# Kernel optimization log

Measured on AMD Instinct MI355X. Metric: run time of the kernel, lower is better.

## Reference

```python
import jax, jax.numpy as jnp
import numpy as np
import math

HEAD = 4
D_MODEL = 128
N_NODES = 2048
SEQ_LEN = 1
D_K = D_MODEL // HEAD
BATCH = 64


def conv1x1_relu(x, w, b):
    # x: [B, C, N, L], w: [O, C], b: [O]  (1x1 Conv2d + ReLU; dropout is identity in eval)
    return jax.nn.relu(jnp.einsum('oc,bcnl->bonl', w, x) + b[None, :, None, None])


def setup_inputs() -> dict:
    key = jax.random.key(0)
    ks = jax.random.split(key, 12)
    s = 0.05
    return {
        'x': jax.random.normal(ks[0], (BATCH, D_MODEL, N_NODES, SEQ_LEN), jnp.float32),
        'q_w': jax.random.normal(ks[1], (D_MODEL, D_MODEL), jnp.float32) * s,
        'q_b': jnp.zeros((D_MODEL,), jnp.float32),
        'v_w': jax.random.normal(ks[2], (D_MODEL, D_MODEL), jnp.float32) * s,
        'v_b': jnp.zeros((D_MODEL,), jnp.float32),
        'c_w': jax.random.normal(ks[3], (D_MODEL, D_MODEL), jnp.float32) * s,
        'c_b': jnp.zeros((D_MODEL,), jnp.float32),
        'memory': jax.random.normal(ks[4], (HEAD, SEQ_LEN, N_NODES, D_K), jnp.float32) * s,
        'nodevec1': jax.random.normal(ks[5], (N_NODES, 10), jnp.float32),
        'nodevec2': jax.random.normal(ks[6], (10, N_NODES), jnp.float32),
        'weights_pool': jax.random.normal(ks[7], (SEQ_LEN, 3, 3), jnp.float32) * s,
        'bias_pool': jax.random.normal(ks[8], (N_NODES, D_K), jnp.float32) * s,
        'aff_w': jnp.ones((D_MODEL, N_NODES, SEQ_LEN), jnp.float32),
        'aff_b': jnp.zeros((D_MODEL, N_NODES, SEQ_LEN), jnp.float32),
    }


def reference(x, q_w, q_b, v_w, v_b, c_w, c_b, memory, nodevec1, nodevec2,
              weights_pool, bias_pool, aff_w, aff_b):
    B = x.shape[0]
    scale = math.sqrt(D_K)

    query = conv1x1_relu(x, q_w, q_b)
    value = conv1x1_relu(x, v_w, v_b)

    # [B, d_model, N, L] -> [B, h, d_k, N, L] -> [B, h, L, N, d_k]
    def split_heads(t):
        return t.reshape(B, HEAD, D_K, N_NODES, SEQ_LEN).transpose(0, 1, 4, 3, 2)

    query = split_heads(query)
    value = split_heads(value)

    key_ = jax.nn.softmax(memory / scale, axis=-1)      # [h, L, N, d_k]
    query = jax.nn.softmax(query / scale, axis=-1)      # [B, h, L, N, d_k]

    Aapt = jax.nn.softmax(jax.nn.relu(nodevec1 @ nodevec2), axis=-1)  # [N, N]

    kv = jnp.einsum('hlnx,bhlny->bhlxy', key_, value)          # [B,h,L,d_k,d_k]
    attn_qkv = jnp.einsum('bhlnx,bhlxy->bhlny', query, kv)     # [B,h,L,N,d_k]

    weights = jnp.einsum('nm,dio->nio', Aapt, weights_pool)    # [N,3,3]
    bias_dyn = Aapt @ bias_pool                                # [N,d_k]
    attn_dyn = jnp.einsum('bhlnc,nio->bhlnc', value, weights) + bias_dyn[None, None, None, :, :]

    out = attn_qkv + attn_dyn                                  # [B,h,L,N,d_k]
    out = out.transpose(0, 1, 4, 3, 2).reshape(B, D_MODEL, N_NODES, SEQ_LEN)
    out = conv1x1_relu(out, c_w, c_b)

    # num_nodes (2048) not in [170, 358, 5] -> affine-residual branch runs
    out = out * aff_w[None] + aff_b[None] + out
    return out
```

## Files before the change

kernel.cpp:

```cpp
#include <hip/hip_runtime.h>

#define NB 64
#define CH 128
#define NNODE 2048
#define NH 4
#define DKK 32
#define INVS 0.17677669529663687f

typedef __bf16 bf16x8 __attribute__((ext_vector_type(8)));
typedef float f32x4 __attribute__((ext_vector_type(4)));
typedef unsigned short ushort_t;

union U16x8 { uint4 u; bf16x8 b; unsigned short s[8]; };
union U16x4 { uint2 u; unsigned short s[4]; };

__device__ inline bf16x8 as_bf16x8(uint4 u){ U16x8 x; x.u = u; return x.b; }
__device__ inline unsigned short f2b(float f){ __bf16 h = (__bf16)f; return __builtin_bit_cast(unsigned short, h); }
__device__ inline float b2f(unsigned short u){ __bf16 h = __builtin_bit_cast(__bf16, u); return (float)h; }

#define SWZ_IDX(n, c) ((n) * 128 + ((c) ^ ((((n) >> 2) & 7) << 3)))

__global__ __launch_bounds__(256) void kA(const float* __restrict__ qw,
    const float* __restrict__ vw, const float* __restrict__ cw,
    const float* __restrict__ memory, const float* __restrict__ bias_pool,
    ushort_t* __restrict__ wqb, ushort_t* __restrict__ wvb, ushort_t* __restrict__ wcb,
    ushort_t* __restrict__ keysT, float* __restrict__ bias_dyn,
    ushort_t* __restrict__ bpT,
    const float* __restrict__ nv1, const float* __restrict__ nv2,
    ushort_t* __restrict__ Ebuf)
{
  __shared__ float red[4];
  int tid = threadIdx.x;
  if (blockIdx.x < 256) {
    int gid = blockIdx.x * 256 + tid;
    if (gid < 16384) { wqb[gid] = f2b(qw[gid]); wvb[gid] = f2b(vw[gid]); wcb[gid] = f2b(cw[gid]); }
    bias_dyn[gid] = 0.f;
    { int k = gid >> 11, m = gid & 2047;
      bpT[gid] = f2b(bias_pool[m * 32 + k]); }
    if (gid < 8192) {
      int h = gid >> 11, n = gid & 2047;
      const float* src = memory + (size_t)gid * 32;
      float v[32]; float m = -1e30f;
      #pragma unroll
      for (int i = 0; i < 32; ++i) { v[i] = src[i] * INVS; m = fmaxf(m, v[i]); }
      float s = 0.f;
      #pragma unroll
      for (int i = 0; i < 32; ++i) { v[i] = __expf(v[i] - m); s += v[i]; }
      float inv = 1.f / s;
      #pragma unroll
      for (int i = 0; i < 32; ++i)
        keysT[(size_t)(h * 32 + i) * 2048 + n] = f2b(v[i] * inv);
    }
  } else {
    int n = blockIdx.x - 256;
    float a1[10];
    #pragma unroll
    for (int d = 0; d < 10; ++d) a1[d] = nv1[n * 10 + d];
    int m0 = tid * 8;
    float s[8];
    #pragma unroll
    for (int j = 0; j < 8; ++j) s[j] = 0.f;
    #pragma unroll
    for (int d = 0; d < 10; ++d) {
      const float* p = nv2 + d * 2048 + m0;
      float4 u = *(const float4*)p; float4 v = *(const float4*)(p + 4);
      s[0] += a1[d] * u.x; s[1] += a1[d] * u.y; s[2] += a1[d] * u.z; s[3] += a1[d] * u.w;
      s[4] += a1[d] * v.x; s[5] += a1[d] * v.y; s[6] += a1[d] * v.z; s[7] += a1[d] * v.w;
    }
    float e[8]; float sum = 0.f;
    #pragma unroll
    for (int j = 0; j < 8; ++j) { e[j] = __expf(fmaxf(s[j], 0.f)); sum += e[j]; }
    #pragma unroll
    for (int d = 1; d < 64; d <<= 1) sum += __shfl_xor(sum, d);
    if ((tid & 63) == 0) red[tid >> 6] = sum;
    __syncthreads();
    float inv = 1.f / (red[0] + red[1] + red[2] + red[3]);
    U16x8 o;
    #pragma unroll
    for (int j = 0; j < 8; ++j) o.s[j] = f2b(e[j] * inv);
    *(uint4*)(Ebuf + (size_t)n * 2048 + m0) = o.u;
  }
}

__global__ __launch_bounds__(256, 5) void kB(
    const ushort_t* __restrict__ Ebuf, const ushort_t* __restrict__ bpT,
    float* __restrict__ bias_dyn,
    const float* __restrict__ x,
    const ushort_t* __restrict__ wqb, const ushort_t* __restrict__ wvb,
    const float* __restrict__ qbias, const float* __restrict__ vbias,
    const ushort_t* __restrict__ keysT,
    ushort_t* __restrict__ QsT, ushort_t* __restrict__ VT,
    float* __restrict__ kvp)
{
  __shared__ __align__(16) ushort_t XT[64 * 128];
  __shared__ __align__(16) ushort_t QO[64 * 128];
  int tid = threadIdx.x; int wv = tid >> 6; int lane = tid & 63;
  int quad = lane >> 4; int l16 = lane & 15;
  f32x4 zero4 = {0.f,0.f,0.f,0.f};

  if (blockIdx.x < 128) {
    int bid = blockIdx.x;
    int n0 = (bid >> 3) * 128;
    int m0 = (bid & 7) * 256;
    int r0 = n0 + 32 * wv;
    f32x4 acc[2][2];
    acc[0][0] = zero4; acc[0][1] = zero4; acc[1][0] = zero4; acc[1][1] = zero4;
    for (int ks = 0; ks < 256; ks += 32) {
      int mb = m0 + ks + 8 * quad;
      bf16x8 a0 = *(const bf16x8*)(Ebuf + (size_t)(r0 + l16) * 2048 + mb);
      bf16x8 a1 = *(const bf16x8*)(Ebuf + (size_t)(r0 + 16 + l16) * 2048 + mb);
      bf16x8 b0 = *(const bf16x8*)(bpT + (size_t)l16 * 2048 + mb);
      bf16x8 b1 = *(const bf16x8*)(bpT + (size_t)(16 + l16) * 2048 + mb);
      acc[0][0] = __builtin_amdgcn_mfma_f32_16x16x32_bf16(a0, b0, acc[0][0], 0, 0, 0);
      acc[0][1] = __builtin_amdgcn_mfma_f32_16x16x32_bf16(a0, b1, acc[0][1], 0, 0, 0);
      acc[1][0] = __builtin_amdgcn_mfma_f32_16x16x32_bf16(a1, b0, acc[1][0], 0, 0, 0);
      acc[1][1] = __builtin_amdgcn_mfma_f32_16x16x32_bf16(a1, b1, acc[1][1], 0, 0, 0);
    }
    #pragma unroll
    for (int rt = 0; rt < 2; ++rt)
      #pragma unroll
      for (int ct = 0; ct < 2; ++ct)
        #pragma unroll
        for (int r = 0; r < 4; ++r)
          atomicAdd(bias_dyn + (size_t)(r0 + 16*rt + 4*quad + r) * 32 + 16*ct + l16,
                    acc[rt][ct][r]);
    return;
  }

  int bid = blockIdx.x - 128; int b = bid >> 5; int n0 = (bid & 31) * 64;

  uint4 wq[2][4];
  #pragma unroll
  for (int ct = 0; ct < 2; ++ct)
    #pragma unroll
    for (int k0 = 0; k0 < 4; ++k0)
      wq[ct][k0] = *(const uint4*)(wqb + (32 * wv + 16 * ct + l16) * 128 + 32 * k0 + 8 * quad);

  {
    float4 r[8];
    int n4 = 4 * (tid & 15);
    #pragma unroll
    for (int p = 0; p < 2; ++p) {
      int c4 = 4 * ((tid >> 4) + 16 * p);
      #pragma unroll
      for (int j = 0; j < 4; ++j)
        r[4 * p + j] = *(const float4*)(x + (size_t)(b * 128 + c4 + j) * 2048 + n0 + n4);
    }
    #pragma unroll
    for (int p = 0; p < 2; ++p) {
      int c4 = 4 * ((tid >> 4) + 16 * p);
      #pragma unroll
      for (int i = 0; i < 4; ++i) {
        U16x4 w;
        w.s[0] = f2b(((const float*)&r[4 * p + 0])[i]);
        w.s[1] = f2b(((const float*)&r[4 * p + 1])[i]);
        w.s[2] = f2b(((const float*)&r[4 * p + 2])[i]);
        w.s[3] = f2b(((const float*)&r[4 * p + 3])[i]);
        *(uint2*)&XT[SWZ_IDX(n4 + i, c4)] = w.u;
      }
    }
  }
  __syncthreads();

  {
    float4 qb4[2];
    #pragma unroll
    for (int ct = 0; ct < 2; ++ct)
      qb4[ct] = *(const float4*)(qbias + 32 * wv + 16 * ct + 4 * quad);
    #pragma unroll
    for (int nt = 0; nt < 4; ++nt) {
      f32x4 aq[2]; aq[0] = zero4; aq[1] = zero4;
      #pragma unroll
      for (int k0 = 0; k0 < 4; ++k0) {
        bf16x8 bfrag = *(const bf16x8*)&XT[SWZ_IDX(16 * nt + l16, 32 * k0 + 8 * quad)];
        aq[0] = __builtin_amdgcn_mfma_f32_16x16x32_bf16(as_bf16x8(wq[0][k0]), bfrag, aq[0], 0, 0, 0);
        aq[1] = __builtin_amdgcn_mfma_f32_16x16x32_bf16(as_bf16x8(wq[1][k0]), bfrag, aq[1], 0, 0, 0);
      }
      float sq[2][4]; float sum = 0.f;
      #pragma unroll
      for (int ct = 0; ct < 2; ++ct)
        #pragma unroll
        for (int r = 0; r < 4; ++r) {
          sq[ct][r] = __expf(fmaxf(aq[ct][r] + ((const float*)&qb4[ct])[r], 0.f) * INVS);
          sum += sq[ct][r];
        }
      sum += __shfl_xor(sum, 16);
      sum += __shfl_xor(sum, 32);
      float inv = 1.f / sum;
      #pragma unroll
      for (int ct = 0; ct < 2; ++ct) {
        U16x4 w;
        #pragma unroll
        for (int r = 0; r < 4; ++r) w.s[r] = f2b(sq[ct][r] * inv);
        *(uint2*)&QO[SWZ_IDX(16 * nt + l16, 32 * wv + 16 * ct + 4 * quad)] = w.u;
      }
    }
  }

  uint2 vout[4][2];
  {
    uint4 wvw[2][4];
    #pragma unroll
    for (int ct = 0; ct < 2; ++ct)
      #pragma unroll
      for (int k0 = 0; k0 < 4; ++k0)
        wvw[ct][k0] = *(const uint4*)(wvb + (32 * wv + 16 * ct + l16) * 128 + 32 * k0 + 8 * quad);
    float4 vb4[2];
    #pragma unroll
    for (int ct = 0; ct < 2; ++ct)
      vb4[ct] = *(const float4*)(vbias + 32 * wv + 16 * ct + 4 * quad);
    #pragma unroll
    for (int nt = 0; nt < 4; ++nt) {
      f32x4 av[2]; av[0] = zero4; av[1] = zero4;
      #pragma unroll
      for (int k0 = 0; k0 < 4; ++k0) {
        bf16x8 bfrag = *(const bf16x8*)&XT[SWZ_IDX(16 * nt + l16, 32 * k0 + 8 * quad)];
        av[0] = __builtin_amdgcn_mfma_f32_16x16x32_bf16(as_bf16x8(wvw[0][k0]), bfrag, av[0], 0, 0, 0);
        av[1] = __builtin_amdgcn_mfma_f32_16x16x32_bf16(as_bf16x8(wvw[1][k0]), bfrag, av[1], 0, 0, 0);
      }
      #pragma unroll
      for (int ct = 0; ct < 2; ++ct) {
        U16x4 w;
        #pragma unroll
        for (int r = 0; r < 4; ++r)
          w.s[r] = f2b(fmaxf(av[ct][r] + ((const float*)&vb4[ct])[r], 0.f));
        vout[nt][ct] = w.u;
      }
    }
  }
  __syncthreads();

  #pragma unroll
  for (int nt = 0; nt < 4; ++nt)
    #pragma unroll
    for (int ct = 0; ct < 2; ++ct)
      *(uint2*)&XT[SWZ_IDX(16 * nt + l16, 32 * wv + 16 * ct + 4 * quad)] = vout[nt][ct];
  __syncthreads();

  {
    f32x4 akv[2][2];
    akv[0][0] = zero4; akv[0][1] = zero4; akv[1][0] = zero4; akv[1][1] = zero4;
    #pragma unroll
    for (int ks = 0; ks < 2; ++ks) {
      const ushort_t* kp = keysT + (size_t)(32 * wv) * 2048 + n0 + 32 * ks + 8 * quad;
      bf16x8 ka0 = *(const bf16x8*)(kp + (size_t)l16 * 2048);
      bf16x8 ka1 = *(const bf16x8*)(kp + (size_t)(16 + l16) * 2048);
      U16x8 v0, v1;
      #pragma unroll
      for (int j = 0; j < 8; ++j) {
        int rowk = 32 * ks + 8 * quad + j;
        v0.s[j] = XT[SWZ_IDX(rowk, 32 * wv + l16)];
        v1.s[j] = XT[SWZ_IDX(rowk, 32 * wv + 16 + l16)];
      }
      akv[0][0] = __builtin_amdgcn_mfma_f32_16x16x32_bf16(ka0, v0.b, akv[0][0], 0, 0, 0);
      akv[0][1] = __builtin_amdgcn_mfma_f32_16x16x32_bf16(ka0, v1.b, akv[0][1], 0, 0, 0);
      akv[1][0] = __builtin_amdgcn_mfma_f32_16x16x32_bf16(ka1, v0.b, akv[1][0], 0, 0, 0);
      akv[1][1] = __builtin_amdgcn_mfma_f32_16x16x32_bf16(ka1, v1.b, akv[1][1], 0, 0, 0);
    }
    float* kdst = kvp + (size_t)bid * 4096 + wv * 1024;
    #pragma unroll
    for (int xt = 0; xt < 2; ++xt)
      #pragma unroll
      for (int yt = 0; yt < 2; ++yt)
        #pragma unroll
        for (int r = 0; r < 4; ++r)
          kdst[(16 * yt + l16) * 32 + 16 * xt + 4 * quad + r] = akv[xt][yt][r];
  }

  #pragma unroll
  for (int j = 0; j < 4; ++j) {
    int id = tid + 256 * j; int n = id >> 4; int u = id & 15;
    size_t go = (size_t)(b * 2048 + n0 + n) * 128 + 8 * u;
    *(uint4*)(QsT + go) = *(uint4*)&QO[SWZ_IDX(n, 8 * u)];
    *(uint4*)(VT  + go) = *(uint4*)&XT[SWZ_IDX(n, 8 * u)];
  }
}

__global__ __launch_bounds__(256) void kred(const float* __restrict__ kvp,
    float* __restrict__ kvws)
{
  int gid = blockIdx.x * 256 + threadIdx.x;
  int b = gid >> 10; int i = gid & 1023;
  const float* p = kvp + (size_t)(b * 32) * 4096 + i * 4;
  float4 s = {0.f,0.f,0.f,0.f};
  #pragma unroll
  for (int t = 0; t < 32; ++t) {
    float4 v = *(const float4*)(p + (size_t)t * 4096);
    s.x += v.x; s.y += v.y; s.z += v.z; s.w += v.w;
  }
  *(float4*)(kvws + (size_t)gid * 4) = s;
}

__global__ __launch_bounds__(256, 4) void k3_out(const ushort_t* __restrict__ QsT,
    const ushort_t* __restrict__ VT, const float* __restrict__ kvws,
    const float* __restrict__ bias_dyn, const ushort_t* __restrict__ wcb,
    const float* __restrict__ cbias, const float* __restrict__ wpool,
    const float* __restrict__ aff_w, const float* __restrict__ aff_b,
    float* __restrict__ out)
{
  int bid = blockIdx.x; int b = bid >> 5; int n0 = (bid & 31) * 64;
  int tid = threadIdx.x; int wv = tid >> 6; int lane = tid & 63;
  int quad = lane >> 4; int l16 = lane & 15;
  __shared__ __align__(16) char smem[37888];
  ushort_t* MID = (ushort_t*)smem;
  ushort_t* VL  = (ushort_t*)(smem + 16384);
  ushort_t (*BD)[40] = (ushort_t(*)[40])(smem + 32768);
  float    (*OST)[64] = (float(*)[64])smem;

  float4 kvlo[2], kvhi[2];
  #pragma unroll
  for (int ct = 0; ct < 2; ++ct) {
    const float* kp = kvws + (size_t)b * 4096 + wv * 1024 + (16 * ct + l16) * 32 + 8 * quad;
    kvlo[ct] = *(const float4*)kp;
    kvhi[ct] = *(const float4*)(kp + 4);
  }
  uint4 aqv[4];
  #pragma unroll
  for (int nt = 0; nt < 4; ++nt)
    aqv[nt] = *(const uint4*)(QsT + (size_t)(b * 2048 + n0 + 16 * nt + l16) * 128 + 32 * wv + 8 * quad);

  float Ws = 0.f;
  #pragma unroll
  for (int i = 0; i < 9; ++i) Ws += wpool[i];

  #pragma unroll
  for (int p = 0; p < 4; ++p) {
    int id = tid + 256 * p; int n = id >> 4; int u = id & 15;
    *(uint4*)&VL[SWZ_IDX(n, 8 * u)] =
        *(const uint4*)(VT + (size_t)(b * 2048 + n0 + n) * 128 + 8 * u);
  }
  #pragma unroll
  for (int p = 0; p < 2; ++p) {
    int id = tid + 256 * p; int n = id >> 3; int g = id & 7;
    float4 v = *(const float4*)(bias_dyn + (size_t)(n0 + n) * 32 + 4 * g);
    U16x4 w;
    w.s[0] = f2b(v.x); w.s[1] = f2b(v.y); w.s[2] = f2b(v.z); w.s[3] = f2b(v.w);
    *(uint2*)&BD[n][4 * g] = w.u;
  }
  U16x8 kf[2];
  #pragma unroll
  for (int ct = 0; ct < 2; ++ct)
    #pragma unroll
    for (int j = 0; j < 4; ++j) {
      kf[ct].s[j]     = f2b(((const float*)&kvlo[ct])[j]);
      kf[ct].s[4 + j] = f2b(((const float*)&kvhi[ct])[j]);
    }
  __syncthreads();

  f32x4 zero4 = {0.f,0.f,0.f,0.f};
  f32x4 acc1[4][2];
  #pragma unroll
  for (int nt = 0; nt < 4; ++nt) { acc1[nt][0] = zero4; acc1[nt][1] = zero4; }
  #pragma unroll
  for (int nt = 0; nt < 4; ++nt)
    #pragma unroll
    for (int ct = 0; ct < 2; ++ct)
      acc1[nt][ct] = __builtin_amdgcn_mfma_f32_16x16x32_bf16(
          as_bf16x8(aqv[nt]), kf[ct].b, acc1[nt][ct], 0, 0, 0);

  uint4 wc[2][4];
  #pragma unroll
  for (int mt = 0; mt < 2; ++mt)
    #pragma unroll
    for (int k0 = 0; k0 < 4; ++k0)
      wc[mt][k0] = *(const uint4*)(wcb + (32 * wv + 16 * mt + l16) * 128 + 32 * k0 + 8 * quad);

  #pragma unroll
  for (int nt = 0; nt < 4; ++nt)
    #pragma unroll
    for (int ct = 0; ct < 2; ++ct)
      #pragma unroll
      for (int r = 0; r < 4; ++r) {
        int nl = 16 * nt + 4 * quad + r;
        int cc = 32 * wv + 16 * ct + l16;
        float v = b2f(VL[SWZ_IDX(nl, cc)]);
        float bd = b2f(BD[nl][16 * ct + l16]);
        MID[SWZ_IDX(nl, cc)] = f2b(acc1[nt][ct][r] + Ws * v + bd);
      }
  __syncthreads();

  f32x4 acc2[2][4];
  #pragma unroll
  for (int mt = 0; mt < 2; ++mt)
    #pragma unroll
    for (int nt = 0; nt < 4; ++nt) acc2[mt][nt] = zero4;
  #pragma unroll
  for (int k0 = 0; k0 < 4; ++k0) {
    bf16x8 bb[4];
    #pragma unroll
    for (int nt = 0; nt < 4; ++nt)
      bb[nt] = *(const bf16x8*)&MID[SWZ_IDX(16 * nt + l16, 32 * k0 + 8 * quad)];
    #pragma unroll
    for (int mt = 0; mt < 2; ++mt)
      #pragma unroll
      for (int nt = 0; nt < 4; ++nt)
        acc2[mt][nt] = __builtin_amdgcn_mfma_f32_16x16x32_bf16(
            as_bf16x8(wc[mt][k0]), bb[nt], acc2[mt][nt], 0, 0, 0);
  }
  __syncthreads();

  float4 cb4[2];
  #pragma unroll
  for (int mt = 0; mt < 2; ++mt)
    cb4[mt] = *(const float4*)(cbias + 32 * wv + 16 * mt + 4 * quad);
  #pragma unroll
  for (int mt = 0; mt < 2; ++mt)
    #pragma unroll
    for (int nt = 0; nt < 4; ++nt)
      #pragma unroll
      for (int r = 0; r < 4; ++r) {
        int c_out = 32 * wv + 16 * mt + 4 * quad + r;
        OST[c_out][16 * nt + l16] = fmaxf(acc2[mt][nt][r] + ((const float*)&cb4[mt])[r], 0.f);
      }
  __syncthreads();

  #pragma unroll
  for (int p = 0; p < 8; ++p) {
    int id = tid + 256 * p; int c = id >> 4; int g = id & 15;
    float4 y = *(const float4*)&OST[c][4 * g];
    size_t ai = (size_t)c * 2048 + n0 + 4 * g;
    float4 aw4 = *(const float4*)(aff_w + ai);
    float4 ab4 = *(const float4*)(aff_b + ai);
    float4 o;
    o.x = y.x * aw4.x + ab4.x + y.x;
    o.y = y.y * aw4.y + ab4.y + y.y;
    o.z = y.z * aw4.z + ab4.z + y.z;
    o.w = y.w * aw4.w + ab4.w + y.w;
    *(float4*)(out + (size_t)(b * 128 + c) * 2048 + n0 + 4 * g) = o;
  }
}

extern "C" void kernel_launch(void* const* d_in, const int* in_sizes, int n_in,
                              void* d_out, int out_size, void* d_ws, size_t ws_size,
                              hipStream_t stream)
{
  const float* x      = (const float*)d_in[0];
  const float* qw     = (const float*)d_in[1];
  const float* qb     = (const float*)d_in[2];
  const float* vw     = (const float*)d_in[3];
  const float* vb     = (const float*)d_in[4];
  const float* cw     = (const float*)d_in[5];
  const float* cb     = (const float*)d_in[6];
  const float* memory = (const float*)d_in[7];
  const float* nv1    = (const float*)d_in[8];
  const float* nv2    = (const float*)d_in[9];
  const float* wpool  = (const float*)d_in[10];
  const float* bpool  = (const float*)d_in[11];
  const float* aw     = (const float*)d_in[12];
  const float* ab     = (const float*)d_in[13];
  float* out = (float*)d_out;

  char* ws = (char*)d_ws;
  ushort_t* QsT      = (ushort_t*)(ws);
  ushort_t* VT       = (ushort_t*)(ws + 33554432);
  float*    kvws     = (float*)   (ws + 67108864);
  ushort_t* keysT    = (ushort_t*)(ws + 68157440);
  float*    bias_dyn = (float*)   (ws + 69206016);
  ushort_t* wqb      = (ushort_t*)(ws + 69468160);
  ushort_t* wvb      = (ushort_t*)(ws + 69500928);
  ushort_t* wcb      = (ushort_t*)(ws + 69533696);
  ushort_t* Ebuf     = (ushort_t*)(ws + 69566464);
  ushort_t* bpT      = (ushort_t*)(ws + 77955072);
  float*    kvp      = (float*)   (ws + 78086144);

  kA<<<2304, 256, 0, stream>>>(qw, vw, cw, memory, bpool, wqb, wvb, wcb,
                               keysT, bias_dyn, bpT, nv1, nv2, Ebuf);
  kB<<<2176, 256, 0, stream>>>(Ebuf, bpT, bias_dyn, x, wqb, wvb, qb, vb,
                               keysT, QsT, VT, kvp);
  kred<<<256, 256, 0, stream>>>(kvp, kvws);
  k3_out<<<2048, 256, 0, stream>>>(QsT, VT, kvws, bias_dyn, wcb, cb, wpool, aw, ab, out);
}
```

Before: 207.5 us.

## Stage x and VT tiles into LDS via direct global_load_lds DMA

Replaces the register-staged load, bf16 convert and transposed LDS store of the x tile in kB with direct global-to-LDS 16-byte loads into an fp32 swizzled buffer. The bf16 conversion moves into the MFMA operand gather, which now reads eight scalar floats per fragment. The VT tile load in k3_out also uses direct-to-LDS DMA. The fp32 staging buffer doubles kB's LDS use, so launch bounds drop from 5 to 3 waves of blocks, lowering occupancy, and per-element LDS reads and conversions are repeated for both the Q and V projections.

```diff
diff --git a/kernel.cpp b/kernel.cpp
--- a/kernel.cpp
+++ b/kernel.cpp
@@ -17,6 +17,12 @@
 __device__ inline bf16x8 as_bf16x8(uint4 u){ U16x8 x; x.u = u; return x.b; }
 __device__ inline unsigned short f2b(float f){ __bf16 h = (__bf16)f; return __builtin_bit_cast(unsigned short, h); }
 __device__ inline float b2f(unsigned short u){ __bf16 h = __builtin_bit_cast(__bf16, u); return (float)h; }
+
+typedef const __attribute__((address_space(1))) void* gas_t;
+typedef __attribute__((address_space(3))) void* las_t;
+__device__ inline void dma16(const void* g, void* l) {
+  __builtin_amdgcn_global_load_lds((gas_t)g, (las_t)l, 16, 0, 0);
+}
 
 #define SWZ_IDX(n, c) ((n) * 128 + ((c) ^ ((((n) >> 2) & 7) << 3)))
 
@@ -82,7 +88,7 @@
   }
 }
 
-__global__ __launch_bounds__(256, 5) void kB(
+__global__ __launch_bounds__(256, 3) void kB(
     const ushort_t* __restrict__ Ebuf, const ushort_t* __restrict__ bpT,
     float* __restrict__ bias_dyn,
     const float* __restrict__ x,
@@ -92,7 +98,7 @@
     ushort_t* __restrict__ QsT, ushort_t* __restrict__ VT,
     float* __restrict__ kvp)
 {
-  __shared__ __align__(16) ushort_t XT[64 * 128];
+  __shared__ __align__(16) float    XS[128 * 64];
   __shared__ __align__(16) ushort_t QO[64 * 128];
   int tid = threadIdx.x; int wv = tid >> 6; int lane = tid & 63;
   int quad = lane >> 4; int l16 = lane & 15;
@@ -129,71 +135,58 @@
 
   int bid = blockIdx.x - 128; int b = bid >> 5; int n0 = (bid & 31) * 64;
 
+  #pragma unroll
+  for (int i = 0; i < 8; ++i) {
+    int k = wv * 8 + i;
+    int c = 4 * k + (lane >> 4);
+    int nsw = ((lane & 15) * 4) ^ (c & 24);
+    dma16(x + (size_t)(b * 128 + c) * 2048 + n0 + nsw, (char*)XS + k * 1024);
+  }
+
   uint4 wq[2][4];
   #pragma unroll
   for (int ct = 0; ct < 2; ++ct)
     #pragma unroll
     for (int k0 = 0; k0 < 4; ++k0)
       wq[ct][k0] = *(const uint4*)(wqb + (32 * wv + 16 * ct + l16) * 128 + 32 * k0 + 8 * quad);
-
-  {
-    float4 r[8];
-    int n4 = 4 * (tid & 15);
-    #pragma unroll
-    for (int p = 0; p < 2; ++p) {
-      int c4 = 4 * ((tid >> 4) + 16 * p);
-      #pragma unroll
-      for (int j = 0; j < 4; ++j)
-        r[4 * p + j] = *(const float4*)(x + (size_t)(b * 128 + c4 + j) * 2048 + n0 + n4);
-    }
-    #pragma unroll
-    for (int p = 0; p < 2; ++p) {
-      int c4 = 4 * ((tid >> 4) + 16 * p);
-      #pragma unroll
-      for (int i = 0; i < 4; ++i) {
-        U16x4 w;
-        w.s[0] = f2b(((const float*)&r[4 * p + 0])[i]);
-        w.s[1] = f2b(((const float*)&r[4 * p + 1])[i]);
-        w.s[2] = f2b(((const float*)&r[4 * p + 2])[i]);
-        w.s[3] = f2b(((const float*)&r[4 * p + 3])[i]);
-        *(uint2*)&XT[SWZ_IDX(n4 + i, c4)] = w.u;
-      }
-    }
-  }
-  __syncthreads();
-
-  {
-    float4 qb4[2];
+  float4 qb4[2], vb4[2];
+  #pragma unroll
+  for (int ct = 0; ct < 2; ++ct) {
+    qb4[ct] = *(const float4*)(qbias + 32 * wv + 16 * ct + 4 * quad);
+    vb4[ct] = *(const float4*)(vbias + 32 * wv + 16 * ct + 4 * quad);
+  }
+  __syncthreads();
+
+  #pragma unroll
+  for (int nt = 0; nt < 4; ++nt) {
+    int nsw = (16 * nt + l16) ^ (8 * quad);
+    f32x4 aq[2]; aq[0] = zero4; aq[1] = zero4;
+    #pragma unroll
+    for (int k0 = 0; k0 < 4; ++k0) {
+      U16x8 u;
+      #pragma unroll
+      for (int j = 0; j < 8; ++j)
+        u.s[j] = f2b(XS[(32 * k0 + 8 * quad + j) * 64 + nsw]);
+      aq[0] = __builtin_amdgcn_mfma_f32_16x16x32_bf16(as_bf16x8(wq[0][k0]), u.b, aq[0], 0, 0, 0);
+      aq[1] = __builtin_amdgcn_mfma_f32_16x16x32_bf16(as_bf16x8(wq[1][k0]), u.b, aq[1], 0, 0, 0);
+    }
+    float sq[2][4]; float sum = 0.f;
     #pragma unroll
     for (int ct = 0; ct < 2; ++ct)
-      qb4[ct] = *(const float4*)(qbias + 32 * wv + 16 * ct + 4 * quad);
-    #pragma unroll
-    for (int nt = 0; nt < 4; ++nt) {
-      f32x4 aq[2]; aq[0] = zero4; aq[1] = zero4;
-      #pragma unroll
-      for (int k0 = 0; k0 < 4; ++k0) {
-        bf16x8 bfrag = *(const bf16x8*)&XT[SWZ_IDX(16 * nt + l16, 32 * k0 + 8 * quad)];
-        aq[0] = __builtin_amdgcn_mfma_f32_16x16x32_bf16(as_bf16x8(wq[0][k0]), bfrag, aq[0], 0, 0, 0);
-        aq[1] = __builtin_amdgcn_mfma_f32_16x16x32_bf16(as_bf16x8(wq[1][k0]), bfrag, aq[1], 0, 0, 0);
-      }
-      float sq[2][4]; float sum = 0.f;
-      #pragma unroll
-      for (int ct = 0; ct < 2; ++ct)
-        #pragma unroll
-        for (int r = 0; r < 4; ++r) {
-          sq[ct][r] = __expf(fmaxf(aq[ct][r] + ((const float*)&qb4[ct])[r], 0.f) * INVS);
-          sum += sq[ct][r];
-        }
-      sum += __shfl_xor(sum, 16);
-      sum += __shfl_xor(sum, 32);
-      float inv = 1.f / sum;
-      #pragma unroll
-      for (int ct = 0; ct < 2; ++ct) {
-        U16x4 w;
-        #pragma unroll
-        for (int r = 0; r < 4; ++r) w.s[r] = f2b(sq[ct][r] * inv);
-        *(uint2*)&QO[SWZ_IDX(16 * nt + l16, 32 * wv + 16 * ct + 4 * quad)] = w.u;
-      }
+      #pragma unroll
+      for (int r = 0; r < 4; ++r) {
+        sq[ct][r] = __expf(fmaxf(aq[ct][r] + ((const float*)&qb4[ct])[r], 0.f) * INVS);
+        sum += sq[ct][r];
+      }
+    sum += __shfl_xor(sum, 16);
+    sum += __shfl_xor(sum, 32);
+    float inv = 1.f / sum;
+    #pragma unroll
+    for (int ct = 0; ct < 2; ++ct) {
+      U16x4 w;
+      #pragma unroll
+      for (int r = 0; r < 4; ++r) w.s[r] = f2b(sq[ct][r] * inv);
+      *(uint2*)&QO[SWZ_IDX(16 * nt + l16, 32 * wv + 16 * ct + 4 * quad)] = w.u;
     }
   }
 
@@ -205,18 +198,18 @@
       #pragma unroll
       for (int k0 = 0; k0 < 4; ++k0)
         wvw[ct][k0] = *(const uint4*)(wvb + (32 * wv + 16 * ct + l16) * 128 + 32 * k0 + 8 * quad);
-    float4 vb4[2];
-    #pragma unroll
-    for (int ct = 0; ct < 2; ++ct)
-      vb4[ct] = *(const float4*)(vbias + 32 * wv + 16 * ct + 4 * quad);
     #pragma unroll
     for (int nt = 0; nt < 4; ++nt) {
+      int nsw = (16 * nt + l16) ^ (8 * quad);
       f32x4 av[2]; av[0] = zero4; av[1] = zero4;
       #pragma unroll
       for (int k0 = 0; k0 < 4; ++k0) {
-        bf16x8 bfrag = *(const bf16x8*)&XT[SWZ_IDX(16 * nt + l16, 32 * k0 + 8 * quad)];
-        av[0] = __builtin_amdgcn_mfma_f32_16x16x32_bf16(as_bf16x8(wvw[0][k0]), bfrag, av[0], 0, 0, 0);
-        av[1] = __builtin_amdgcn_mfma_f32_16x16x32_bf16(as_bf16x8(wvw[1][k0]), bfrag, av[1], 0, 0, 0);
+        U16x8 u;
+        #pragma unroll
+        for (int j = 0; j < 8; ++j)
+          u.s[j] = f2b(XS[(32 * k0 + 8 * quad + j) * 64 + nsw]);
+        av[0] = __builtin_amdgcn_mfma_f32_16x16x32_bf16(as_bf16x8(wvw[0][k0]), u.b, av[0], 0, 0, 0);
+        av[1] = __builtin_amdgcn_mfma_f32_16x16x32_bf16(as_bf16x8(wvw[1][k0]), u.b, av[1], 0, 0, 0);
       }
       #pragma unroll
       for (int ct = 0; ct < 2; ++ct) {
@@ -230,11 +223,12 @@
   }
   __syncthreads();
 
+  ushort_t* VL = (ushort_t*)XS;
   #pragma unroll
   for (int nt = 0; nt < 4; ++nt)
     #pragma unroll
     for (int ct = 0; ct < 2; ++ct)
-      *(uint2*)&XT[SWZ_IDX(16 * nt + l16, 32 * wv + 16 * ct + 4 * quad)] = vout[nt][ct];
+      *(uint2*)&VL[SWZ_IDX(16 * nt + l16, 32 * wv + 16 * ct + 4 * quad)] = vout[nt][ct];
   __syncthreads();
 
   {
@@ -249,8 +243,8 @@
       #pragma unroll
       for (int j = 0; j < 8; ++j) {
         int rowk = 32 * ks + 8 * quad + j;
-        v0.s[j] = XT[SWZ_IDX(rowk, 32 * wv + l16)];
-        v1.s[j] = XT[SWZ_IDX(rowk, 32 * wv + 16 + l16)];
+        v0.s[j] = VL[SWZ_IDX(rowk, 32 * wv + l16)];
+        v1.s[j] = VL[SWZ_IDX(rowk, 32 * wv + 16 + l16)];
       }
       akv[0][0] = __builtin_amdgcn_mfma_f32_16x16x32_bf16(ka0, v0.b, akv[0][0], 0, 0, 0);
       akv[0][1] = __builtin_amdgcn_mfma_f32_16x16x32_bf16(ka0, v1.b, akv[0][1], 0, 0, 0);
@@ -272,7 +266,7 @@
     int id = tid + 256 * j; int n = id >> 4; int u = id & 15;
     size_t go = (size_t)(b * 2048 + n0 + n) * 128 + 8 * u;
     *(uint4*)(QsT + go) = *(uint4*)&QO[SWZ_IDX(n, 8 * u)];
-    *(uint4*)(VT  + go) = *(uint4*)&XT[SWZ_IDX(n, 8 * u)];
+    *(uint4*)(VT  + go) = *(uint4*)&VL[SWZ_IDX(n, 8 * u)];
   }
 }
 
@@ -307,6 +301,14 @@
   ushort_t (*BD)[40] = (ushort_t(*)[40])(smem + 32768);
   float    (*OST)[64] = (float(*)[64])smem;
 
+  #pragma unroll
+  for (int i = 0; i < 4; ++i) {
+    int k = wv * 4 + i;
+    int row = 4 * k + (lane >> 4);
+    int col8 = ((lane & 15) * 8) ^ (((row >> 2) & 7) << 3);
+    dma16(VT + (size_t)(b * 2048 + n0 + row) * 128 + col8, (char*)VL + k * 1024);
+  }
+
   float4 kvlo[2], kvhi[2];
   #pragma unroll
   for (int ct = 0; ct < 2; ++ct) {
@@ -323,12 +325,6 @@
   #pragma unroll
   for (int i = 0; i < 9; ++i) Ws += wpool[i];
 
-  #pragma unroll
-  for (int p = 0; p < 4; ++p) {
-    int id = tid + 256 * p; int n = id >> 4; int u = id & 15;
-    *(uint4*)&VL[SWZ_IDX(n, 8 * u)] =
-        *(const uint4*)(VT + (size_t)(b * 2048 + n0 + n) * 128 + 8 * u);
-  }
   #pragma unroll
   for (int p = 0; p < 2; ++p) {
     int id = tid + 256 * p; int n = id >> 3; int g = id & 7;
```

New measurement: 319.0 us. 53.7% more time.

## Fuse Aapt@bias_pool into softmax kernel, drop Ebuf round-trip and MFMA blocks

Applied to the files above, without the earlier changes.

Computes bias_dyn = softmax(relu(nv1@nv2)) @ bias_pool directly in the row-softmax blocks of kA, using fp32 FMAs against bias_pool plus a wave shuffle and shared-memory reduction. This removes the 8 MB bf16 Ebuf write and read, the bpT transpose, the zeroing of bias_dyn, the atomics, and the 128 extra MFMA blocks in kB. In exchange each kA row block does 32-wide shuffle reductions (6 x 32 shuffles) and reads bias_pool redundantly, which raises register pressure and ALU work in kA.

```diff
diff --git a/kernel.cpp b/kernel.cpp
--- a/kernel.cpp
+++ b/kernel.cpp
@@ -25,18 +25,14 @@
     const float* __restrict__ memory, const float* __restrict__ bias_pool,
     ushort_t* __restrict__ wqb, ushort_t* __restrict__ wvb, ushort_t* __restrict__ wcb,
     ushort_t* __restrict__ keysT, float* __restrict__ bias_dyn,
-    ushort_t* __restrict__ bpT,
-    const float* __restrict__ nv1, const float* __restrict__ nv2,
-    ushort_t* __restrict__ Ebuf)
+    const float* __restrict__ nv1, const float* __restrict__ nv2)
 {
   __shared__ float red[4];
+  __shared__ float red2[4][32];
   int tid = threadIdx.x;
   if (blockIdx.x < 256) {
     int gid = blockIdx.x * 256 + tid;
     if (gid < 16384) { wqb[gid] = f2b(qw[gid]); wvb[gid] = f2b(vw[gid]); wcb[gid] = f2b(cw[gid]); }
-    bias_dyn[gid] = 0.f;
-    { int k = gid >> 11, m = gid & 2047;
-      bpT[gid] = f2b(bias_pool[m * 32 + k]); }
     if (gid < 8192) {
       int h = gid >> 11, n = gid & 2047;
       const float* src = memory + (size_t)gid * 32;
@@ -75,16 +71,38 @@
     if ((tid & 63) == 0) red[tid >> 6] = sum;
     __syncthreads();
     float inv = 1.f / (red[0] + red[1] + red[2] + red[3]);
-    U16x8 o;
-    #pragma unroll
-    for (int j = 0; j < 8; ++j) o.s[j] = f2b(e[j] * inv);
-    *(uint4*)(Ebuf + (size_t)n * 2048 + m0) = o.u;
+
+    float acc[32];
+    #pragma unroll
+    for (int k = 0; k < 32; ++k) acc[k] = 0.f;
+    const float* bp = bias_pool + (size_t)m0 * 32;
+    #pragma unroll
+    for (int j = 0; j < 8; ++j) {
+      float ej = e[j] * inv;
+      #pragma unroll
+      for (int g = 0; g < 8; ++g) {
+        float4 bv = *(const float4*)(bp + j * 32 + 4 * g);
+        acc[4 * g + 0] += ej * bv.x;
+        acc[4 * g + 1] += ej * bv.y;
+        acc[4 * g + 2] += ej * bv.z;
+        acc[4 * g + 3] += ej * bv.w;
+      }
+    }
+    #pragma unroll
+    for (int d = 1; d < 64; d <<= 1)
+      #pragma unroll
+      for (int k = 0; k < 32; ++k)
+        acc[k] += __shfl_xor(acc[k], d);
+    int wvid = tid >> 6, ln = tid & 63;
+    if (ln < 32) red2[wvid][ln] = acc[ln];
+    __syncthreads();
+    if (tid < 32)
+      bias_dyn[(size_t)n * 32 + tid] =
+          red2[0][tid] + red2[1][tid] + red2[2][tid] + red2[3][tid];
   }
 }
 
 __global__ __launch_bounds__(256, 5) void kB(
-    const ushort_t* __restrict__ Ebuf, const ushort_t* __restrict__ bpT,
-    float* __restrict__ bias_dyn,
     const float* __restrict__ x,
     const ushort_t* __restrict__ wqb, const ushort_t* __restrict__ wvb,
     const float* __restrict__ qbias, const float* __restrict__ vbias,
@@ -98,36 +116,7 @@
   int quad = lane >> 4; int l16 = lane & 15;
   f32x4 zero4 = {0.f,0.f,0.f,0.f};
 
-  if (blockIdx.x < 128) {
-    int bid = blockIdx.x;
-    int n0 = (bid >> 3) * 128;
-    int m0 = (bid & 7) * 256;
-    int r0 = n0 + 32 * wv;
-    f32x4 acc[2][2];
-    acc[0][0] = zero4; acc[0][1] = zero4; acc[1][0] = zero4; acc[1][1] = zero4;
-    for (int ks = 0; ks < 256; ks += 32) {
-      int mb = m0 + ks + 8 * quad;
-      bf16x8 a0 = *(const bf16x8*)(Ebuf + (size_t)(r0 + l16) * 2048 + mb);
-      bf16x8 a1 = *(const bf16x8*)(Ebuf + (size_t)(r0 + 16 + l16) * 2048 + mb);
-      bf16x8 b0 = *(const bf16x8*)(bpT + (size_t)l16 * 2048 + mb);
-      bf16x8 b1 = *(const bf16x8*)(bpT + (size_t)(16 + l16) * 2048 + mb);
-      acc[0][0] = __builtin_amdgcn_mfma_f32_16x16x32_bf16(a0, b0, acc[0][0], 0, 0, 0);
-      acc[0][1] = __builtin_amdgcn_mfma_f32_16x16x32_bf16(a0, b1, acc[0][1], 0, 0, 0);
-      acc[1][0] = __builtin_amdgcn_mfma_f32_16x16x32_bf16(a1, b0, acc[1][0], 0, 0, 0);
-      acc[1][1] = __builtin_amdgcn_mfma_f32_16x16x32_bf16(a1, b1, acc[1][1], 0, 0, 0);
-    }
-    #pragma unroll
-    for (int rt = 0; rt < 2; ++rt)
-      #pragma unroll
-      for (int ct = 0; ct < 2; ++ct)
-        #pragma unroll
-        for (int r = 0; r < 4; ++r)
-          atomicAdd(bias_dyn + (size_t)(r0 + 16*rt + 4*quad + r) * 32 + 16*ct + l16,
-                    acc[rt][ct][r]);
-    return;
-  }
-
-  int bid = blockIdx.x - 128; int b = bid >> 5; int n0 = (bid & 31) * 64;
+  int bid = blockIdx.x; int b = bid >> 5; int n0 = (bid & 31) * 64;
 
   uint4 wq[2][4];
   #pragma unroll
@@ -459,14 +448,11 @@
   ushort_t* wqb      = (ushort_t*)(ws + 69468160);
   ushort_t* wvb      = (ushort_t*)(ws + 69500928);
   ushort_t* wcb      = (ushort_t*)(ws + 69533696);
-  ushort_t* Ebuf     = (ushort_t*)(ws + 69566464);
-  ushort_t* bpT      = (ushort_t*)(ws + 77955072);
   float*    kvp      = (float*)   (ws + 78086144);
 
   kA<<<2304, 256, 0, stream>>>(qw, vw, cw, memory, bpool, wqb, wvb, wcb,
-                               keysT, bias_dyn, bpT, nv1, nv2, Ebuf);
-  kB<<<2176, 256, 0, stream>>>(Ebuf, bpT, bias_dyn, x, wqb, wvb, qb, vb,
-                               keysT, QsT, VT, kvp);
+                               keysT, bias_dyn, nv1, nv2);
+  kB<<<2048, 256, 0, stream>>>(x, wqb, wvb, qb, vb, keysT, QsT, VT, kvp);
   kred<<<256, 256, 0, stream>>>(kvp, kvws);
   k3_out<<<2048, 256, 0, stream>>>(QsT, VT, kvws, bias_dyn, wcb, cb, wpool, aw, ab, out);
 }
```

Result: slower. 301.2 us (+45.2%).
